# Kernel tuning notes

Hardware: AMD Instinct MI355X
Metric: run time of the kernel (lower is better)

## Reference

```python
import jax, jax.numpy as jnp
import numpy as np

H = 768      # hidden_size (MambaConfig default)
DI = 500     # intermediate_size (overridden)
N = 16       # state_size
R = 48       # time_step_rank = ceil(768/16)
K = 4        # conv_kernel
LYR = 5      # num_hidden_layers
EPS = 1e-5   # layer_norm_epsilon
B, L, IN = 8, 1024, 4096


def _rmsnorm(x, w):
    v = jnp.mean(jnp.square(x), axis=-1, keepdims=True)
    return x * jax.lax.rsqrt(v + EPS) * w


def _mixer(x, in_proj, conv_w, conv_b, x_proj, dt_w, dt_b, A_log, Dp, out_w):
    # x: [B, L, H]
    proj = x @ in_proj                       # [B, L, 2*DI]
    u, gate = jnp.split(proj, 2, axis=-1)
    # causal depthwise conv1d (torch Conv1d padding=K-1, sliced to L)
    up = jnp.pad(u, ((0, 0), (K - 1, 0), (0, 0)))
    conv = conv_b
    for k in range(K):
        conv = conv + up[:, k:k + x.shape[1], :] * conv_w[:, k]
    u = jax.nn.silu(conv)                    # [B, L, DI]
    ssm = u @ x_proj                         # [B, L, R + 2N]
    dt, Bm, Cm = ssm[..., :R], ssm[..., R:R + N], ssm[..., R + N:]
    dt = jax.nn.softplus(dt @ dt_w + dt_b)   # [B, L, DI]
    A = -jnp.exp(A_log)                      # [DI, N]
    dA = jnp.exp(dt[..., None] * A)          # [B, L, DI, N]
    dBu = dt[..., None] * Bm[:, :, None, :] * u[..., None]  # [B, L, DI, N]

    def step(h, xs):
        dA_t, dBu_t, C_t = xs
        h = dA_t * h + dBu_t                 # [B, DI, N]
        y = jnp.einsum('bdn,bn->bd', h, C_t)
        return h, y

    h0 = jnp.zeros((u.shape[0], DI, N), dtype=u.dtype)
    _, ys = jax.lax.scan(step, h0, (dA.transpose(1, 0, 2, 3),
                                    dBu.transpose(1, 0, 2, 3),
                                    Cm.transpose(1, 0, 2)))
    y = ys.transpose(1, 0, 2)                # [B, L, DI]
    y = y + u * Dp
    y = y * jax.nn.silu(gate)
    return y @ out_w                         # [B, L, H]


def setup_inputs() -> dict:
    key = jax.random.key(0)
    ks = jax.random.split(key, 12)
    s = 0.02
    inputs = jax.random.normal(ks[0], (B, L, IN), jnp.float32)
    W_down = jax.random.normal(ks[1], (IN, H), jnp.float32) * s
    in_proj = jax.random.normal(ks[2], (LYR, H, 2 * DI), jnp.float32) * s
    conv_w = jax.random.normal(ks[3], (LYR, DI, K), jnp.float32) * 0.1
    conv_b = jnp.zeros((LYR, DI), jnp.float32)
    x_proj = jax.random.normal(ks[4], (LYR, DI, R + 2 * N), jnp.float32) * s
    dt_w = jax.random.normal(ks[5], (LYR, R, DI), jnp.float32) * s
    dt_b = jax.random.normal(ks[6], (LYR, DI), jnp.float32) * 0.1
    A_log = jnp.broadcast_to(jnp.log(jnp.arange(1, N + 1, dtype=jnp.float32)),
                             (LYR, DI, N)).copy()
    D_param = jnp.ones((LYR, DI), jnp.float32)
    out_w = jax.random.normal(ks[7], (LYR, DI, H), jnp.float32) * s
    norm_w = jnp.ones((LYR, H), jnp.float32)
    norm_f_w = jnp.ones((H,), jnp.float32)
    W_cls = jax.random.normal(ks[8], (H, 1), jnp.float32) * s
    return dict(inputs=inputs, W_down=W_down, in_proj=in_proj, conv_w=conv_w,
                conv_b=conv_b, x_proj=x_proj, dt_w=dt_w, dt_b=dt_b,
                A_log=A_log, D_param=D_param, out_w=out_w, norm_w=norm_w,
                norm_f_w=norm_f_w, W_cls=W_cls)


def reference(inputs, W_down, in_proj, conv_w, conv_b, x_proj, dt_w, dt_b,
              A_log, D_param, out_w, norm_w, norm_f_w, W_cls):
    x = inputs @ W_down                      # down projection [B, L, H]
    for i in range(LYR):
        x = x + _mixer(_rmsnorm(x, norm_w[i]), in_proj[i], conv_w[i],
                       conv_b[i], x_proj[i], dt_w[i], dt_b[i], A_log[i],
                       D_param[i], out_w[i])
    x = _rmsnorm(x, norm_f_w)
    out = x[:, -1]                           # last token [B, H]
    logits = out @ W_cls                     # [B, 1]
    return logits
```

## Files before the change

kernel.cpp:

```cpp
#include <hip/hip_runtime.h>
#include <hip/hip_bf16.h>

#define BATCH 8
#define SEQL 1024
#define INDIM 4096
#define HDIM 768
#define DI 500
#define NSTATE 16
#define RRANK 48
#define KCONV 4
#define NLAYER 5
#define BL (BATCH * SEQL)

typedef __attribute__((ext_vector_type(8))) short bf16x8;
typedef __attribute__((ext_vector_type(4))) float f32x4;

__device__ __forceinline__ void gl_lds16(const void* g, void* l) {
  __builtin_amdgcn_global_load_lds(
      (const __attribute__((address_space(1))) void*)g,
      (__attribute__((address_space(3))) void*)l, 16, 0, 0);
}

__device__ __forceinline__ unsigned short f2bf(float v) {
  return __hip_bfloat16_raw(__float2bfloat16(v)).x;
}
__device__ __forceinline__ float bf2f(unsigned short h) {
  unsigned int u = ((unsigned int)h) << 16;
  float f;
  memcpy(&f, &u, 4);
  return f;
}

template <int EPI>
__global__ __launch_bounds__(256) void gemm_mfma(
    const short* __restrict__ A, const short* __restrict__ Bt,
    float* __restrict__ C, const float* __restrict__ bias,
    unsigned short* __restrict__ D0, unsigned short* __restrict__ D1,
    int M, int N, int K, int lda, int ldb, int ldc) {
  __shared__ short As[2][128 * 32];
  __shared__ short Bs[2][128 * 32];
  const int tid = threadIdx.x;
  const int w = tid >> 6, lane = tid & 63;
  const int m0 = blockIdx.y * 128, n0 = blockIdx.x * 128;
  const int wr = w >> 1, wc = w & 1;
  f32x4 acc[4][4] = {};

  const int srow = tid >> 2;
  const int cpos = tid & 3;
  const int sc = (cpos ^ ((srow >> 1) & 3)) * 8;
  const short* ga0 = A + (size_t)(m0 + srow) * lda + sc;
  const short* ga1 = A + (size_t)(m0 + 64 + srow) * lda + sc;
  const short* gb0 = Bt + (size_t)(n0 + srow) * ldb + sc;
  const short* gb1 = Bt + (size_t)(n0 + 64 + srow) * ldb + sc;
  const int lr = lane & 15, kb = lane >> 4;
  const int kbx = (kb ^ ((lr >> 1) & 3)) * 8;

  auto stage = [&](int buf, int k0) {
    gl_lds16(ga0 + k0, &As[buf][w * 512]);
    gl_lds16(ga1 + k0, &As[buf][2048 + w * 512]);
    gl_lds16(gb0 + k0, &Bs[buf][w * 512]);
    gl_lds16(gb1 + k0, &Bs[buf][2048 + w * 512]);
  };
  auto compute = [&](int buf) {
    bf16x8 af[4], bfr[4];
#pragma unroll
    for (int i = 0; i < 4; ++i) {
      af[i] = *(const bf16x8*)&As[buf][(wr * 64 + i * 16 + lr) * 32 + kbx];
      bfr[i] = *(const bf16x8*)&Bs[buf][(wc * 64 + i * 16 + lr) * 32 + kbx];
    }
#pragma unroll
    for (int i = 0; i < 4; ++i)
#pragma unroll
      for (int j = 0; j < 4; ++j)
        acc[i][j] = __builtin_amdgcn_mfma_f32_16x16x32_bf16(af[i], bfr[j],
                                                            acc[i][j], 0, 0, 0);
  };

  const int nk = K >> 5;
  stage(0, 0);
  __syncthreads();
  int cur = 0;
  for (int t = 0; t < nk - 1; ++t) {
    stage(cur ^ 1, (t + 1) * 32);
    compute(cur);
    __syncthreads();
    cur ^= 1;
  }
  compute(cur);

#pragma unroll
  for (int i = 0; i < 4; ++i) {
    const int row = m0 + wr * 64 + i * 16 + (lane >> 4) * 4;
#pragma unroll
    for (int j = 0; j < 4; ++j) {
      const int col = n0 + wc * 64 + j * 16 + (lane & 15);
      if (EPI == 3) {
        if (col < N) {
          float4 v4;
#pragma unroll
          for (int r = 0; r < 4; ++r) {
            float v = acc[i][j][r] + bias[col];
            ((float*)&v4)[r] = (v > 15.f) ? v : log1pf(expf(v));
          }
          const int bb = row >> 10, tt = row & 1023;
          *(float4*)&C[((size_t)bb * DI + col) * 1024 + tt] = v4;
        }
      } else if (EPI == 4) {
#pragma unroll
        for (int r = 0; r < 4; ++r) {
          unsigned short h = f2bf(acc[i][j][r]);
          size_t rr = (size_t)(row + r);
          if (col < DI)
            D0[rr * 512 + col] = h;
          else
            D1[rr * 512 + (col - DI)] = h;
        }
      } else if (EPI == 5) {
#pragma unroll
        for (int r = 0; r < 4; ++r) {
          float v = acc[i][j][r];
          size_t rr = (size_t)(row + r);
          if (col < N) C[rr * ldc + col] = v;
          if (col < 64) D0[rr * 64 + col] = f2bf(col < RRANK ? v : 0.f);
        }
      } else {
        if (col < N) {
#pragma unroll
          for (int r = 0; r < 4; ++r) {
            float v = acc[i][j][r];
            size_t idx = (size_t)(row + r) * ldc + col;
            if (EPI == 1) v += C[idx];
            C[idx] = v;
          }
        }
      }
    }
  }
}

__global__ __launch_bounds__(256) void convert_cast(
    const float* __restrict__ src, __hip_bfloat16* __restrict__ dst, long n) {
  long i = ((long)blockIdx.x * 256 + threadIdx.x) * 4;
  if (i >= n) return;
  float4 v = *(const float4*)(src + i);
  dst[i + 0] = __float2bfloat16(v.x);
  dst[i + 1] = __float2bfloat16(v.y);
  dst[i + 2] = __float2bfloat16(v.z);
  dst[i + 3] = __float2bfloat16(v.w);
}

__global__ __launch_bounds__(256) void convert_wT(
    const float* __restrict__ src, __hip_bfloat16* __restrict__ dst, int K,
    int N, int Kpad, int Npad, long src_lstride, long dst_lstride) {
  int idx = blockIdx.x * 256 + threadIdx.x;
  int per = Kpad * Npad;
  if (idx >= per) return;
  const float* s = src + (long)blockIdx.y * src_lstride;
  __hip_bfloat16* d = dst + (long)blockIdx.y * dst_lstride;
  int n = idx / Kpad, k = idx % Kpad;
  float v = (k < K && n < N) ? s[(long)k * N + n] : 0.f;
  d[idx] = __float2bfloat16(v);
}

__device__ __forceinline__ float block_sum256(float v, float* sm) {
#pragma unroll
  for (int off = 32; off > 0; off >>= 1) v += __shfl_down(v, off, 64);
  int wid = threadIdx.x >> 6;
  if ((threadIdx.x & 63) == 0) sm[wid] = v;
  __syncthreads();
  float t = sm[0] + sm[1] + sm[2] + sm[3];
  __syncthreads();
  return t;
}

__global__ __launch_bounds__(256) void rmsnorm_kernel(
    const float* __restrict__ X, const float* __restrict__ w,
    __hip_bfloat16* __restrict__ XN) {
  __shared__ float sm[4];
  const long row = blockIdx.x;
  const float* x = X + row * HDIM;
  float vals[3];
  float s = 0.f;
#pragma unroll
  for (int j = 0; j < 3; ++j) {
    vals[j] = x[threadIdx.x + j * 256];
    s += vals[j] * vals[j];
  }
  float tot = block_sum256(s, sm);
  float scale = rsqrtf(tot / (float)HDIM + 1e-5f);
#pragma unroll
  for (int j = 0; j < 3; ++j) {
    int c = threadIdx.x + j * 256;
    XN[row * HDIM + c] = __float2bfloat16(vals[j] * scale * w[c]);
  }
}

__global__ __launch_bounds__(256) void conv_fused_kernel(
    const unsigned short* __restrict__ Uraw, const float* __restrict__ cw,
    const float* __restrict__ cb, unsigned short* __restrict__ Ubf,
    unsigned short* __restrict__ Ut, int layer) {
  __shared__ unsigned short tin[35][33];
  __shared__ unsigned short tout[32][33];
  const int d0 = blockIdx.x * 32, t0 = blockIdx.y * 32, b = blockIdx.z;
  const int tx = threadIdx.x & 31, ty = threadIdx.x >> 5;
#pragma unroll
  for (int r = 0; r < 5; ++r) {
    int tr = ty + r * 8;
    if (tr < 35) {
      int t = t0 + tr - (KCONV - 1);
      tin[tr][tx] =
          (t >= 0) ? Uraw[((size_t)b * 1024 + t) * 512 + d0 + tx] : 0;
    }
  }
  __syncthreads();
  const int d = d0 + tx;
  float w0 = 0.f, w1 = 0.f, w2 = 0.f, w3 = 0.f, bias = 0.f;
  if (d < DI) {
    const float* w = cw + ((size_t)layer * DI + d) * KCONV;
    w0 = w[0]; w1 = w[1]; w2 = w[2]; w3 = w[3];
    bias = cb[layer * DI + d];
  }
#pragma unroll
  for (int r = 0; r < 4; ++r) {
    const int tt = ty + r * 8;
    unsigned short h = 0;
    if (d < DI) {
      float a = bias + w0 * bf2f(tin[tt][tx]) + w1 * bf2f(tin[tt + 1][tx]) +
                w2 * bf2f(tin[tt + 2][tx]) + w3 * bf2f(tin[tt + 3][tx]);
      h = f2bf(a / (1.f + expf(-a)));
    }
    tout[tt][tx] = h;
    Ubf[((size_t)b * 1024 + t0 + tt) * 512 + d] = h;
  }
  __syncthreads();
#pragma unroll
  for (int r = 0; r < 4; ++r) {
    const int dd = ty + r * 8;
    Ut[((size_t)b * 512 + d0 + dd) * 1024 + t0 + tx] = tout[tx][dd];
  }
}

__global__ __launch_bounds__(256) void y_gate_kernel(
    const unsigned short* __restrict__ Yt, const unsigned short* __restrict__ G,
    unsigned short* __restrict__ Ybf) {
  __shared__ unsigned short tile[32][33];
  const int d0 = blockIdx.x * 32, t0 = blockIdx.y * 32, b = blockIdx.z;
  const int tx = threadIdx.x & 31, ty = threadIdx.x >> 5;
#pragma unroll
  for (int r = 0; r < 4; ++r) {
    int d = d0 + ty + r * 8;
    tile[ty + r * 8][tx] =
        (d < DI) ? Yt[((size_t)b * 512 + d) * 1024 + t0 + tx]
                 : (unsigned short)0;
  }
  __syncthreads();
#pragma unroll
  for (int r = 0; r < 4; ++r) {
    size_t row = (size_t)b * 1024 + t0 + ty + r * 8;
    int d = d0 + tx;
    float yv = 0.f;
    if (d < DI) {
      float y = bf2f(tile[tx][ty + r * 8]);
      float g = bf2f(G[row * 512 + d]);
      yv = y * (g / (1.f + expf(-g)));
    }
    Ybf[row * 512 + d] = f2bf(yv);
  }
}

__global__ __launch_bounds__(256) void scan_kernel(
    const float* __restrict__ DTt, const unsigned short* __restrict__ Ut,
    const float* __restrict__ SSM, const float* __restrict__ A_log,
    const float* __restrict__ Dparam, unsigned short* __restrict__ Yt,
    int layer) {
  __shared__ float sdt[1040];
  __shared__ float su[1040];
  __shared__ float s_ap[16][17];
  __shared__ float s_h0[16][17];
  __shared__ float s_hi[16][17];
  const int blk = blockIdx.x;
  const int b = blk / DI, d = blk % DI;
  const int tid = threadIdx.x;
  const int c = tid >> 4, n = tid & 15;

  const float* dtp = DTt + ((size_t)b * DI + d) * 1024;
  const unsigned short* up = Ut + ((size_t)b * 512 + d) * 1024;
#pragma unroll
  for (int k = 0; k < 4; ++k) {
    int x = tid + k * 256;
    sdt[x + (x >> 6)] = dtp[x];
    su[x + (x >> 6)] = bf2f(up[x]);
  }
  __syncthreads();

  const float An = -expf(A_log[((size_t)layer * DI + d) * NSTATE + n]);
  const float Dp = Dparam[layer * DI + d];
  const int t0 = c * 64;
  const int sb = t0 + c;
  const float* ssmB = SSM + ((size_t)b * 1024 + t0) * 128 + RRANK + n;

  float h = 0.f, ap = 1.f;
  for (int s = 0; s < 64; ++s) {
    float dt = sdt[sb + s];
    float a = __expf(dt * An);
    h = a * h + dt * su[sb + s] * ssmB[(size_t)s * 128];
    ap *= a;
  }
  s_ap[c][n] = ap;
  s_h0[c][n] = h;
  __syncthreads();

  if (tid < 16) {
    float hi = 0.f;
    for (int cc = 0; cc < 16; ++cc) {
      s_hi[cc][tid] = hi;
      hi = s_ap[cc][tid] * hi + s_h0[cc][tid];
    }
  }
  __syncthreads();

  h = s_hi[c][n];
  unsigned short* yp = Yt + ((size_t)b * 512 + d) * 1024 + t0;
  for (int s = 0; s < 64; ++s) {
    float dt = sdt[sb + s];
    float u = su[sb + s];
    float a = __expf(dt * An);
    h = a * h + dt * u * ssmB[(size_t)s * 128];
    float p = h * ssmB[(size_t)s * 128 + 16];
    p += __shfl_xor(p, 1, 64);
    p += __shfl_xor(p, 2, 64);
    p += __shfl_xor(p, 4, 64);
    p += __shfl_xor(p, 8, 64);
    if (n == 0) {
      float y = p + u * Dp;
      yp[s] = f2bf(y);
    }
  }
}

__global__ __launch_bounds__(256) void final_kernel(
    const float* __restrict__ X, const float* __restrict__ nfw,
    const float* __restrict__ Wcls, float* __restrict__ out) {
  __shared__ float sm[4];
  const int b = blockIdx.x;
  const long row = (long)b * SEQL + (SEQL - 1);
  const float* x = X + row * HDIM;
  float vals[3];
  float s = 0.f;
#pragma unroll
  for (int j = 0; j < 3; ++j) {
    vals[j] = x[threadIdx.x + j * 256];
    s += vals[j] * vals[j];
  }
  float tot = block_sum256(s, sm);
  float scale = rsqrtf(tot / (float)HDIM + 1e-5f);
  float dot = 0.f;
#pragma unroll
  for (int j = 0; j < 3; ++j) {
    int c = threadIdx.x + j * 256;
    dot += vals[j] * scale * nfw[c] * Wcls[c];
  }
  float td = block_sum256(dot, sm);
  if (threadIdx.x == 0) out[b] = td;
}

extern "C" void kernel_launch(void* const* d_in, const int* in_sizes, int n_in,
                              void* d_out, int out_size, void* d_ws,
                              size_t ws_size, hipStream_t stream) {
  const float* inputs  = (const float*)d_in[0];
  const float* W_down  = (const float*)d_in[1];
  const float* in_proj = (const float*)d_in[2];
  const float* conv_w  = (const float*)d_in[3];
  const float* conv_b  = (const float*)d_in[4];
  const float* x_proj  = (const float*)d_in[5];
  const float* dt_w    = (const float*)d_in[6];
  const float* dt_b    = (const float*)d_in[7];
  const float* A_log   = (const float*)d_in[8];
  const float* D_param = (const float*)d_in[9];
  const float* out_w   = (const float*)d_in[10];
  const float* norm_w  = (const float*)d_in[11];
  const float* norm_fw = (const float*)d_in[12];
  const float* W_cls   = (const float*)d_in[13];
  float* out = (float*)d_out;

  char* ws = (char*)d_ws;
  __hip_bfloat16* Abf   = (__hip_bfloat16*)(ws + 0);
  __hip_bfloat16* Wdbf  = (__hip_bfloat16*)(ws + 67108864);
  __hip_bfloat16* XNbf  = (__hip_bfloat16*)(ws + 0);
  unsigned short* Yt    = (unsigned short*)(ws + 0);
  float*          DTt   = (float*)(ws + 12582912);
  unsigned short* Uraw  = (unsigned short*)(ws + 28966912);
  unsigned short* Ybf   = (unsigned short*)(ws + 28966912);
  unsigned short* Gate  = (unsigned short*)(ws + 37355520);
  unsigned short* Ubf   = (unsigned short*)(ws + 45744128);
  unsigned short* Ut    = (unsigned short*)(ws + 54132736);
  float*          SSM   = (float*)(ws + 62521344);
  __hip_bfloat16* SSMbf = (__hip_bfloat16*)(ws + 66715648);
  float*          X     = (float*)(ws + 73400320);
  __hip_bfloat16* inpbf = (__hip_bfloat16*)(ws + 98566144);
  __hip_bfloat16* xpbf  = (__hip_bfloat16*)(ws + 106430464);
  __hip_bfloat16* dtwbf = (__hip_bfloat16*)(ws + 107085824);
  __hip_bfloat16* outwbf= (__hip_bfloat16*)(ws + 107413504);

  convert_cast<<<(long)BL * 4096 / 4 / 256, 256, 0, stream>>>(inputs, Abf,
                                                              (long)BL * 4096);
  convert_wT<<<dim3((768 * 4096 + 255) / 256, 1), 256, 0, stream>>>(
      W_down, Wdbf, 4096, 768, 4096, 768, 0, 0);
  convert_wT<<<dim3((768 * 1024 + 255) / 256, NLAYER), 256, 0, stream>>>(
      in_proj, inpbf, 768, 1000, 768, 1024, (long)HDIM * 1000, 768 * 1024);
  convert_wT<<<dim3((128 * 512 + 255) / 256, NLAYER), 256, 0, stream>>>(
      x_proj, xpbf, 500, 80, 512, 128, (long)DI * 80, 128 * 512);
  convert_wT<<<dim3((512 * 64 + 255) / 256, NLAYER), 256, 0, stream>>>(
      dt_w, dtwbf, 48, 500, 64, 512, (long)RRANK * DI, 512 * 64);
  convert_wT<<<dim3((768 * 512 + 255) / 256, NLAYER), 256, 0, stream>>>(
      out_w, outwbf, 500, 768, 512, 768, (long)DI * HDIM, 768 * 512);

  gemm_mfma<0><<<dim3(768 / 128, BL / 128), 256, 0, stream>>>(
      (const short*)Abf, (const short*)Wdbf, X, nullptr, nullptr, nullptr, BL,
      HDIM, INDIM, INDIM, INDIM, HDIM);

  for (int i = 0; i < NLAYER; ++i) {
    rmsnorm_kernel<<<BL, 256, 0, stream>>>(X, norm_w + i * HDIM, XNbf);
    gemm_mfma<4><<<dim3(1024 / 128, BL / 128), 256, 0, stream>>>(
        (const short*)XNbf, (const short*)(inpbf + (long)i * 768 * 1024),
        nullptr, nullptr, Uraw, Gate, BL, 1000, HDIM, HDIM, HDIM, 0);
    conv_fused_kernel<<<dim3(16, 32, 8), 256, 0, stream>>>(Uraw, conv_w,
                                                           conv_b, Ubf, Ut, i);
    gemm_mfma<5><<<dim3(1, BL / 128), 256, 0, stream>>>(
        (const short*)Ubf, (const short*)(xpbf + (long)i * 128 * 512), SSM,
        nullptr, (unsigned short*)SSMbf, nullptr, BL, 80, 512, 512, 512, 128);
    gemm_mfma<3><<<dim3(512 / 128, BL / 128), 256, 0, stream>>>(
        (const short*)SSMbf, (const short*)(dtwbf + (long)i * 512 * 64), DTt,
        dt_b + i * DI, nullptr, nullptr, BL, DI, 64, 64, 64, 0);
    scan_kernel<<<BATCH * DI, 256, 0, stream>>>(DTt, Ut, SSM, A_log, D_param,
                                                Yt, i);
    y_gate_kernel<<<dim3(16, 32, 8), 256, 0, stream>>>(Yt, Gate, Ybf);
    gemm_mfma<1><<<dim3(768 / 128, BL / 128), 256, 0, stream>>>(
        (const short*)Ybf, (const short*)(outwbf + (long)i * 768 * 512), X,
        nullptr, nullptr, nullptr, BL, HDIM, 512, 512, 512, HDIM);
  }

  final_kernel<<<BATCH, 256, 0, stream>>>(X, norm_fw, W_cls, out);
}
```

Measured before the change: 1.265 ms.

## Triple-buffer GEMM LDS pipeline and remap workgroups across XCDs

The bf16 MFMA GEMM moves from a double-buffered LDS pipeline to a three-stage one. Explicit vmcnt waits and a single barrier per k-step let loads for step t+2 stay in flight while step t is computed. Workgroup IDs in both the GEMM and the scan kernel are remapped so that consecutive logical tiles land on the same XCD, aiming for better L2 locality. The extra LDS buffer raises shared memory per block and may reduce occupancy. The remap assumes the total workgroup count divides by 8, which holds for the scan grid (4000) but may not for every GEMM grid, in which case the permutation would break.

Result: faster. 1.158 ms (-8.5%).

```diff
diff --git a/kernel.cpp b/kernel.cpp
--- a/kernel.cpp
+++ b/kernel.cpp
@@ -37,11 +37,17 @@
     float* __restrict__ C, const float* __restrict__ bias,
     unsigned short* __restrict__ D0, unsigned short* __restrict__ D1,
     int M, int N, int K, int lda, int ldb, int ldc) {
-  __shared__ short As[2][128 * 32];
-  __shared__ short Bs[2][128 * 32];
+  __shared__ short As[3][128 * 32];
+  __shared__ short Bs[3][128 * 32];
   const int tid = threadIdx.x;
   const int w = tid >> 6, lane = tid & 63;
-  const int m0 = blockIdx.y * 128, n0 = blockIdx.x * 128;
+
+  const int gx = gridDim.x;
+  const int nwg = gx * gridDim.y;
+  int flat = blockIdx.y * gx + blockIdx.x;
+  flat = (flat & 7) * (nwg >> 3) + (flat >> 3);
+  const int m0 = (flat / gx) * 128, n0 = (flat % gx) * 128;
+
   const int wr = w >> 1, wc = w & 1;
   f32x4 acc[4][4] = {};
 
@@ -78,15 +84,24 @@
 
   const int nk = K >> 5;
   stage(0, 0);
-  __syncthreads();
+  if (nk > 1) stage(1, 32);
   int cur = 0;
-  for (int t = 0; t < nk - 1; ++t) {
-    stage(cur ^ 1, (t + 1) * 32);
+  for (int t = 0; t < nk; ++t) {
+    if (t + 1 < nk)
+      asm volatile("s_waitcnt vmcnt(4)" ::: "memory");
+    else
+      asm volatile("s_waitcnt vmcnt(0)" ::: "memory");
+    __builtin_amdgcn_s_barrier();
+    __builtin_amdgcn_sched_barrier(0);
     compute(cur);
-    __syncthreads();
-    cur ^= 1;
-  }
-  compute(cur);
+    if (t + 2 < nk) {
+      int nb = cur + 2;
+      if (nb >= 3) nb -= 3;
+      stage(nb, (t + 2) * 32);
+    }
+    ++cur;
+    if (cur == 3) cur = 0;
+  }
 
 #pragma unroll
   for (int i = 0; i < 4; ++i) {
@@ -278,7 +293,8 @@
   __shared__ float s_ap[16][17];
   __shared__ float s_h0[16][17];
   __shared__ float s_hi[16][17];
-  const int blk = blockIdx.x;
+  const int orig = blockIdx.x;
+  const int blk = (orig & 7) * (BATCH * DI / 8) + (orig >> 3);
   const int b = blk / DI, d = blk % DI;
   const int tid = threadIdx.x;
   const int c = tid >> 4, n = tid & 15;
```
